# Kernel optimization log

Measured on AMD Instinct MI355X. Metric: run time of the kernel, lower is better.

Reference implementation:

```python
import jax, jax.numpy as jnp
import numpy as np

B, S, H, NH = 8, 1024, 1024, 16
HD = H // NH  # head dim = 64

def setup_inputs() -> dict:
    key = jax.random.key(0)
    ks = jax.random.split(key, 7)
    sc = 0.02
    return {
        "activation": jax.random.normal(ks[0], (B, S, H), jnp.float32),
        "qw": jax.random.normal(ks[1], (H, H), jnp.float32) * sc,
        "qb": jax.random.normal(ks[2], (H,), jnp.float32) * sc,
        "kw": jax.random.normal(ks[3], (H, H), jnp.float32) * sc,
        "kb": jax.random.normal(ks[4], (H,), jnp.float32) * sc,
        "vw": jax.random.normal(ks[5], (H, H), jnp.float32) * sc,
        "vb": jax.random.normal(ks[6], (H,), jnp.float32) * sc,
    }

def reference(activation, qw, qb, kw, kb, vw, vb):
    # QKV projections (torch Linear: x @ W^T + b)
    def proj(x, w, b):
        y = jnp.einsum('bsh,oh->bso', x, w) + b
        # split heads: [B,S,H] -> [B,NH,S,HD]
        return y.reshape(B, S, NH, HD).transpose(0, 2, 1, 3)
    q = proj(activation, qw, qb)
    k = proj(activation, kw, kb)
    v = proj(activation, vw, vb)
    # NOTE: source scales by 1/sqrt(hidden_dim), NOT 1/sqrt(head_dim)
    scale = 1.0 / jnp.sqrt(jnp.float32(H))
    scores = jnp.einsum('bnqd,bnkd->bnqk', q, k) * scale
    probs = jax.nn.softmax(scores, axis=-1)
    ctx = jnp.einsum('bnqk,bnkd->bnqd', probs, v)
    # merge heads: [B,NH,S,HD] -> [B,S,H]
    return ctx.transpose(0, 2, 1, 3).reshape(B, S, H)
```

## Files before the change

kernel.cpp:

```cpp
#include <hip/hip_runtime.h>
#include <cstdint>
#include <cstddef>

#define B_   8
#define S_   1024
#define H_   1024
#define NH_  16
#define HD_  64
#define M_   8192
#define N3_  3072
#define K_   1024

typedef __attribute__((ext_vector_type(8))) short bf16x8;
typedef __attribute__((ext_vector_type(4))) float f32x4;
typedef __attribute__((ext_vector_type(16))) float f32x16;
typedef __attribute__((ext_vector_type(8))) unsigned short u16x8;
typedef __attribute__((ext_vector_type(4))) unsigned u32x4;

__device__ __forceinline__ unsigned short f2bf(float f) {
  unsigned u = __builtin_bit_cast(unsigned, f);
  u += 0x7fffu + ((u >> 16) & 1u);
  return (unsigned short)(u >> 16);
}

__device__ __forceinline__ unsigned cvtpk(float a, float b) {
  unsigned r;
  asm("v_cvt_pk_bf16_f32 %0, %1, %2" : "=v"(r) : "v"(a), "v"(b));
  return r;
}

__global__ void cvt_kernel(const float* __restrict__ src,
                           unsigned short* __restrict__ dst, int n) {
  const int stride = gridDim.x * blockDim.x * 8;
  for (int i = (blockIdx.x * blockDim.x + threadIdx.x) * 8; i < n; i += stride) {
    float4 a = *reinterpret_cast<const float4*>(src + i);
    float4 b = *reinterpret_cast<const float4*>(src + i + 4);
    u16x8 o;
    o[0] = f2bf(a.x); o[1] = f2bf(a.y); o[2] = f2bf(a.z); o[3] = f2bf(a.w);
    o[4] = f2bf(b.x); o[5] = f2bf(b.y); o[6] = f2bf(b.z); o[7] = f2bf(b.w);
    *reinterpret_cast<u16x8*>(dst + i) = o;
  }
}

#define BM 128
#define BN 128
#define BK 64

__global__ __launch_bounds__(256) void qkv_gemm(
    const unsigned short* __restrict__ A,
    const unsigned short* __restrict__ Bw,
    const float* __restrict__ qb, const float* __restrict__ kb,
    const float* __restrict__ vb,
    unsigned short* __restrict__ Qh,
    unsigned short* __restrict__ Kh,
    unsigned short* __restrict__ Vth)
{
  __shared__ unsigned short As[BM * BK];
  __shared__ unsigned short Bs[BN * BK];
  const int t = threadIdx.x;
  const int lane = t & 63;
  const int bm = blockIdx.x, bn = blockIdx.y;
  const int wm = t >> 7, wn = (t >> 6) & 1;

  f32x4 acc[4][4] = {};

  const char* Ab = (const char*)(A + (size_t)bm * BM * K_);
  const char* Bb = (const char*)(Bw + (size_t)bn * BN * K_);

  for (int kt = 0; kt < K_ / BK; ++kt) {
    const int k0b = kt * BK * 2;
    #pragma unroll
    for (int i = 0; i < 4; ++i) {
      const int off = (i * 256 + t) * 16;
      const int row = off >> 7;
      const int c16 = (off >> 4) & 7;
      const int sc  = c16 ^ (row & 7);
      __builtin_amdgcn_global_load_lds(
          (const __attribute__((address_space(1))) void*)(Ab + (size_t)row * (K_ * 2) + k0b + sc * 16),
          (__attribute__((address_space(3))) void*)((char*)As + off), 16, 0, 0);
      __builtin_amdgcn_global_load_lds(
          (const __attribute__((address_space(1))) void*)(Bb + (size_t)row * (K_ * 2) + k0b + sc * 16),
          (__attribute__((address_space(3))) void*)((char*)Bs + off), 16, 0, 0);
    }
    __syncthreads();

    #pragma unroll
    for (int kk = 0; kk < 2; ++kk) {
      bf16x8 af[4], bfr[4];
      #pragma unroll
      for (int mb = 0; mb < 4; ++mb) {
        const int row = wm * 64 + mb * 16 + (lane & 15);
        const int j   = kk * 4 + (lane >> 4);
        af[mb] = *reinterpret_cast<const bf16x8*>(
            (const char*)As + row * 128 + ((j ^ (row & 7)) << 4));
      }
      #pragma unroll
      for (int nb = 0; nb < 4; ++nb) {
        const int row = wn * 64 + nb * 16 + (lane & 15);
        const int j   = kk * 4 + (lane >> 4);
        bfr[nb] = *reinterpret_cast<const bf16x8*>(
            (const char*)Bs + row * 128 + ((j ^ (row & 7)) << 4));
      }
      #pragma unroll
      for (int mb = 0; mb < 4; ++mb)
        #pragma unroll
        for (int nb = 0; nb < 4; ++nb)
          acc[mb][nb] = __builtin_amdgcn_mfma_f32_16x16x32_bf16(
              af[mb], bfr[nb], acc[mb][nb], 0, 0, 0);
    }
    __syncthreads();
  }

  const int grow = bm * BM + wm * 64;
  const int gcol = bn * BN + wn * 64;
  #pragma unroll
  for (int nb = 0; nb < 4; ++nb) {
    const int col = gcol + nb * 16 + (lane & 15);
    const int tensor = col >> 10;
    const int o  = col & 1023;
    const int nh = o >> 6, hd = o & 63;
    const float* bias = (tensor == 0) ? qb : (tensor == 1) ? kb : vb;
    const float bv  = bias[o];
    const float scl = (tensor == 0) ? 0.04508422f : 1.0f;
    #pragma unroll
    for (int mb = 0; mb < 4; ++mb) {
      #pragma unroll
      for (int r = 0; r < 4; ++r) {
        const int i  = grow + mb * 16 + (lane >> 4) * 4 + r;
        const int bb = i >> 10, s = i & 1023;
        const unsigned short h = f2bf((acc[mb][nb][r] + bv) * scl);
        const int bhn = bb * NH_ + nh;
        if (tensor == 0)      Qh[((size_t)bhn * S_ + s) * HD_ + hd] = h;
        else if (tensor == 1) Kh[((size_t)bhn * S_ + s) * HD_ + hd] = h;
        else                  Vth[(size_t)bhn * 65536 + (s >> 6) * 4096 + hd * 64 + (s & 63)] = h;
      }
    }
  }
}

__device__ __forceinline__ bf16x8 mk_frag(const f32x16& s, const int base) {
  unsigned a0 = cvtpk(s[base + 0], s[base + 1]);
  unsigned a1 = cvtpk(s[base + 2], s[base + 3]);
  unsigned b0 = cvtpk(s[base + 4], s[base + 5]);
  unsigned b1 = cvtpk(s[base + 6], s[base + 7]);
  asm("v_permlane32_swap_b32 %0, %1" : "+v"(a0), "+v"(b0));
  asm("v_permlane32_swap_b32 %0, %1" : "+v"(a1), "+v"(b1));
  u32x4 u = {a0, a1, b0, b1};
  return __builtin_bit_cast(bf16x8, u);
}

__global__ __launch_bounds__(256, 3) void attn_kernel(
    const unsigned short* __restrict__ Qh,
    const unsigned short* __restrict__ Kh,
    const unsigned short* __restrict__ Vth,
    float* __restrict__ Out)
{
  __shared__ char sm[2][16384];
  const int t = threadIdx.x;
  const int lane = t & 63;
  const int wave = t >> 6;
  const int l31 = lane & 31;
  const int hi = lane >> 5;
  const int hw = blockIdx.x;
  const int xcd = hw & 7;
  const int qt = (hw >> 3) & 7;
  const int bh = (hw >> 6) * 8 + xcd;
  const int b = bh >> 4, nh = bh & 15;

  const unsigned short* Qp = Qh + (size_t)bh * (S_ * HD_);
  const char* Kp = (const char*)Kh + (size_t)bh * 131072;
  const char* Vp = (const char*)Vth + (size_t)bh * 131072;
  const int q0 = qt * 128 + wave * 32;

  bf16x8 bq[4];
  #pragma unroll
  for (int st = 0; st < 4; ++st)
    bq[st] = *reinterpret_cast<const bf16x8*>(
        Qp + (size_t)(q0 + l31) * HD_ + st * 16 + hi * 8);

  const int soff0 = wave * 1024 + lane * 16;
  #define STAGE_TILE(dstbase, srcbase)                                            \
    _Pragma("unroll")                                                             \
    for (int j = 0; j < 2; ++j) {                                                 \
      const int off = j * 4096 + soff0;                                           \
      const int row = off >> 7;                                                   \
      const int sc  = ((off >> 4) & 7) ^ (row & 7);    \
      __builtin_amdgcn_global_load_lds(                                           \
          (const __attribute__((address_space(1))) void*)((srcbase) + row * 128 + sc * 16), \
          (__attribute__((address_space(3))) void*)((dstbase) + off), 16, 0, 0);  \
    }

  STAGE_TILE(&sm[0][0],    Kp)
  STAGE_TILE(&sm[0][8192], Vp)
  __syncthreads();

  f32x16 o0 = {}, o1 = {};
  float lsum = 0.f;
  const int swr = l31 & 7;

  for (int kt = 0; kt < 16; ++kt) {
    const int cur = kt & 1;
    if (kt < 15) {
      STAGE_TILE(&sm[cur ^ 1][0],    Kp + (kt + 1) * 8192)
      STAGE_TILE(&sm[cur ^ 1][8192], Vp + (kt + 1) * 8192)
    }
    const char* Kb = &sm[cur][0];
    const char* Vb = &sm[cur][8192];

    f32x16 s0 = {}, s1 = {};
    #pragma unroll
    for (int st = 0; st < 4; ++st) {
      const int c = ((st * 2 + hi) ^ swr) << 4;
      bf16x8 ka = *reinterpret_cast<const bf16x8*>(Kb + l31 * 128 + c);
      bf16x8 kc = *reinterpret_cast<const bf16x8*>(Kb + (l31 + 32) * 128 + c);
      s0 = __builtin_amdgcn_mfma_f32_32x32x16_bf16(ka, bq[st], s0, 0, 0, 0);
      s1 = __builtin_amdgcn_mfma_f32_32x32x16_bf16(kc, bq[st], s1, 0, 0, 0);
    }

    bf16x8 va[4];
    #pragma unroll
    for (int ks = 0; ks < 2; ++ks) {
      const int c = ((ks * 2 + hi) ^ swr) << 4;
      va[ks * 2]     = *reinterpret_cast<const bf16x8*>(Vb + l31 * 128 + c);
      va[ks * 2 + 1] = *reinterpret_cast<const bf16x8*>(Vb + (l31 + 32) * 128 + c);
    }
    #pragma unroll
    for (int r = 0; r < 16; ++r) {
      s0[r] = __builtin_amdgcn_exp2f(s0[r]);
      lsum += s0[r];
    }
    bf16x8 f0 = mk_frag(s0, 0);
    bf16x8 f1 = mk_frag(s0, 8);
    o0 = __builtin_amdgcn_mfma_f32_32x32x16_bf16(f0, va[0], o0, 0, 0, 0);
    o1 = __builtin_amdgcn_mfma_f32_32x32x16_bf16(f0, va[1], o1, 0, 0, 0);
    o0 = __builtin_amdgcn_mfma_f32_32x32x16_bf16(f1, va[2], o0, 0, 0, 0);
    o1 = __builtin_amdgcn_mfma_f32_32x32x16_bf16(f1, va[3], o1, 0, 0, 0);

    #pragma unroll
    for (int ks = 0; ks < 2; ++ks) {
      const int c = (((ks + 2) * 2 + hi) ^ swr) << 4;
      va[ks * 2]     = *reinterpret_cast<const bf16x8*>(Vb + l31 * 128 + c);
      va[ks * 2 + 1] = *reinterpret_cast<const bf16x8*>(Vb + (l31 + 32) * 128 + c);
    }
    #pragma unroll
    for (int r = 0; r < 16; ++r) {
      s1[r] = __builtin_amdgcn_exp2f(s1[r]);
      lsum += s1[r];
    }
    bf16x8 f2 = mk_frag(s1, 0);
    bf16x8 f3 = mk_frag(s1, 8);
    o0 = __builtin_amdgcn_mfma_f32_32x32x16_bf16(f2, va[0], o0, 0, 0, 0);
    o1 = __builtin_amdgcn_mfma_f32_32x32x16_bf16(f2, va[1], o1, 0, 0, 0);
    o0 = __builtin_amdgcn_mfma_f32_32x32x16_bf16(f3, va[2], o0, 0, 0, 0);
    o1 = __builtin_amdgcn_mfma_f32_32x32x16_bf16(f3, va[3], o1, 0, 0, 0);

    __syncthreads();
  }

  const float ltot = lsum + __shfl_xor(lsum, 32);
  const float inv = 1.0f / ltot;
  #pragma unroll
  for (int r = 0; r < 16; ++r) {
    const int crow = (r & 3) + 8 * (r >> 2) + 4 * hi;
    const float invq = __shfl(inv, crow);
    float* op = Out + ((size_t)(b * S_ + q0 + crow)) * H_ + nh * HD_ + l31;
    op[0]  = o0[r] * invq;
    op[32] = o1[r] * invq;
  }
}

extern "C" void kernel_launch(void* const* d_in, const int* in_sizes, int n_in,
                              void* d_out, int out_size, void* d_ws, size_t ws_size,
                              hipStream_t stream) {
  const float* act = (const float*)d_in[0];
  const float* qw  = (const float*)d_in[1];
  const float* qb  = (const float*)d_in[2];
  const float* kw  = (const float*)d_in[3];
  const float* kb  = (const float*)d_in[4];
  const float* vw  = (const float*)d_in[5];
  const float* vb  = (const float*)d_in[6];

  char* ws = (char*)d_ws;
  unsigned short* actb = (unsigned short*)ws;
  unsigned short* wb   = (unsigned short*)(ws + 16777216);
  unsigned short* Qh   = (unsigned short*)(ws + 23068672);
  unsigned short* Kh   = Qh + 8388608;
  unsigned short* Vth  = Kh + 8388608;

  cvt_kernel<<<4096, 256, 0, stream>>>(act, actb, M_ * K_);
  cvt_kernel<<<512, 256, 0, stream>>>(qw, wb,               H_ * H_);
  cvt_kernel<<<512, 256, 0, stream>>>(kw, wb + 1048576,     H_ * H_);
  cvt_kernel<<<512, 256, 0, stream>>>(vw, wb + 2097152,     H_ * H_);

  dim3 gg(M_ / BM, N3_ / BN);
  qkv_gemm<<<gg, 256, 0, stream>>>(actb, wb, qb, kb, vb, Qh, Kh, Vth);

  attn_kernel<<<1024, 256, 0, stream>>>(Qh, Kh, Vth, (float*)d_out);
}
```

Before: 141.5 us.

## Rewrite QKV GEMM with 256x256 tiles and double-buffered phased LDS pipeline

The QKV projection GEMM moves from 128x128 tiles with single-buffered LDS and 256 threads to 256x256 tiles computed by 512 threads. It uses 128 KB of dynamic LDS with double buffering. Each k-step is split into four sub-phases that interleave global-to-LDS prefetch of the next tile with MFMA on the current one, using explicit vmcnt waits, barriers and s_setprio. A block-index swizzle groups tiles across XCDs for better L2 reuse. This targets load latency that is exposed and the low reuse of small tiles, at the cost of one block per CU and fragile hand-tuned wait counts.

After: 178.1 us. 25.8% more time.

```diff
diff --git a/kernel.cpp b/kernel.cpp
--- a/kernel.cpp
+++ b/kernel.cpp
@@ -42,11 +42,7 @@
   }
 }
 
-#define BM 128
-#define BN 128
-#define BK 64
-
-__global__ __launch_bounds__(256) void qkv_gemm(
+__global__ __launch_bounds__(512, 2) void qkv_gemm(
     const unsigned short* __restrict__ A,
     const unsigned short* __restrict__ Bw,
     const float* __restrict__ qb, const float* __restrict__ kb,
@@ -55,84 +51,129 @@
     unsigned short* __restrict__ Kh,
     unsigned short* __restrict__ Vth)
 {
-  __shared__ unsigned short As[BM * BK];
-  __shared__ unsigned short Bs[BN * BK];
+  extern __shared__ char sm[];
+  char* Asm = sm;
+  char* Bsm = sm + 65536;
+
   const int t = threadIdx.x;
   const int lane = t & 63;
-  const int bm = blockIdx.x, bn = blockIdx.y;
-  const int wm = t >> 7, wn = (t >> 6) & 1;
-
-  f32x4 acc[4][4] = {};
-
-  const char* Ab = (const char*)(A + (size_t)bm * BM * K_);
-  const char* Bb = (const char*)(Bw + (size_t)bn * BN * K_);
-
-  for (int kt = 0; kt < K_ / BK; ++kt) {
-    const int k0b = kt * BK * 2;
-    #pragma unroll
-    for (int i = 0; i < 4; ++i) {
-      const int off = (i * 256 + t) * 16;
-      const int row = off >> 7;
-      const int c16 = (off >> 4) & 7;
-      const int sc  = c16 ^ (row & 7);
-      __builtin_amdgcn_global_load_lds(
-          (const __attribute__((address_space(1))) void*)(Ab + (size_t)row * (K_ * 2) + k0b + sc * 16),
-          (__attribute__((address_space(3))) void*)((char*)As + off), 16, 0, 0);
-      __builtin_amdgcn_global_load_lds(
-          (const __attribute__((address_space(1))) void*)(Bb + (size_t)row * (K_ * 2) + k0b + sc * 16),
-          (__attribute__((address_space(3))) void*)((char*)Bs + off), 16, 0, 0);
-    }
-    __syncthreads();
-
-    #pragma unroll
-    for (int kk = 0; kk < 2; ++kk) {
-      bf16x8 af[4], bfr[4];
+  const int wave = t >> 6;
+  const int wm = wave >> 2;
+  const int wn = wave & 3;
+
+  const int bid = blockIdx.x;
+  const int swz = (bid & 7) * 48 + (bid >> 3);
+  const int bm = swz & 31;
+  const int bn = swz >> 5;
+
+  const char* Ab = (const char*)A + (size_t)bm * 256 * 2048;
+  const char* Bb = (const char*)Bw + (size_t)bn * 256 * 2048;
+
+  f32x4 acc[2][2][4][2] = {};
+
+  #define STG(lbase, gbase, kt, h)                                             \
+    { _Pragma("unroll")                                                        \
+      for (int j = 0; j < 2; ++j) {                                            \
+        const int off = (h) * 16384 + j * 8192 + t * 16;                       \
+        const int row = off >> 7;                                              \
+        const int sc  = ((off >> 4) & 7) ^ (row & 7);                          \
+        __builtin_amdgcn_global_load_lds(                                      \
+          (const __attribute__((address_space(1))) void*)((gbase) + row * 2048 + (kt) * 128 + sc * 16), \
+          (__attribute__((address_space(3))) void*)((lbase) + off), 16, 0, 0); \
+      } }
+
+  #define VM4 asm volatile("s_waitcnt vmcnt(4)" ::: "memory")
+  #define VM2 asm volatile("s_waitcnt vmcnt(2)" ::: "memory")
+  #define VM0 asm volatile("s_waitcnt vmcnt(0)" ::: "memory")
+  #define BAR asm volatile("s_barrier" ::: "memory")
+  #define NOPS
+
+  #define PHASE(MH, NH, STAGE_STMT, WAIT_STMT)                                 \
+  {                                                                            \
+    bf16x8 afr[2][4], bfr[2][2];                                               \
+    _Pragma("unroll")                                                          \
+    for (int ks = 0; ks < 2; ++ks) {                                           \
+      _Pragma("unroll")                                                        \
+      for (int f = 0; f < 4; ++f) {                                            \
+        const int ar = (MH) * 128 + wm * 64 + f * 16 + (lane & 15);            \
+        afr[ks][f] = *(const bf16x8*)(Acur + ar * 128 +                        \
+                      (((ks * 4 + (lane >> 4)) ^ (ar & 7)) << 4));             \
+      }                                                                        \
+      _Pragma("unroll")                                                        \
+      for (int g = 0; g < 2; ++g) {                                            \
+        const int br = (NH) * 128 + wn * 32 + g * 16 + (lane & 15);            \
+        bfr[ks][g] = *(const bf16x8*)(Bcur + br * 128 +                        \
+                      (((ks * 4 + (lane >> 4)) ^ (br & 7)) << 4));             \
+      }                                                                        \
+    }                                                                          \
+    STAGE_STMT;                                                                \
+    WAIT_STMT;                                                                 \
+    BAR;                                                                       \
+    __builtin_amdgcn_s_setprio(1);                                             \
+    _Pragma("unroll")                                                          \
+    for (int ks = 0; ks < 2; ++ks)                                             \
+      _Pragma("unroll")                                                        \
+      for (int f = 0; f < 4; ++f)                                              \
+        _Pragma("unroll")                                                      \
+        for (int g = 0; g < 2; ++g)                                            \
+          acc[MH][NH][f][g] = __builtin_amdgcn_mfma_f32_16x16x32_bf16(         \
+              afr[ks][f], bfr[ks][g], acc[MH][NH][f][g], 0, 0, 0);             \
+    __builtin_amdgcn_s_setprio(0);                                             \
+    BAR;                                                                       \
+  }
+
+  STG(Asm, Ab, 0, 0)
+  STG(Bsm, Bb, 0, 0)
+  STG(Bsm, Bb, 0, 1)
+  STG(Asm, Ab, 0, 1)
+  VM4;
+  BAR;
+
+  for (int kt = 0; kt < 15; ++kt) {
+    const char* Acur = Asm + (kt & 1) * 32768;
+    const char* Bcur = Bsm + (kt & 1) * 32768;
+    char* Anx = Asm + ((kt + 1) & 1) * 32768;
+    char* Bnx = Bsm + ((kt + 1) & 1) * 32768;
+    PHASE(0, 0, STG(Anx, Ab, kt + 1, 0), VM4)
+    PHASE(0, 1, STG(Bnx, Bb, kt + 1, 0), VM4)
+    PHASE(1, 0, STG(Bnx, Bb, kt + 1, 1), NOPS)
+    PHASE(1, 1, STG(Anx, Ab, kt + 1, 1), VM4)
+  }
+  {
+    const char* Acur = Asm + 32768;
+    const char* Bcur = Bsm + 32768;
+    PHASE(0, 0, NOPS, VM2)
+    PHASE(0, 1, NOPS, VM0)
+    PHASE(1, 0, NOPS, NOPS)
+    PHASE(1, 1, NOPS, NOPS)
+  }
+
+  #pragma unroll
+  for (int mh = 0; mh < 2; ++mh) {
+    #pragma unroll
+    for (int nh = 0; nh < 2; ++nh) {
       #pragma unroll
-      for (int mb = 0; mb < 4; ++mb) {
-        const int row = wm * 64 + mb * 16 + (lane & 15);
-        const int j   = kk * 4 + (lane >> 4);
-        af[mb] = *reinterpret_cast<const bf16x8*>(
-            (const char*)As + row * 128 + ((j ^ (row & 7)) << 4));
-      }
-      #pragma unroll
-      for (int nb = 0; nb < 4; ++nb) {
-        const int row = wn * 64 + nb * 16 + (lane & 15);
-        const int j   = kk * 4 + (lane >> 4);
-        bfr[nb] = *reinterpret_cast<const bf16x8*>(
-            (const char*)Bs + row * 128 + ((j ^ (row & 7)) << 4));
-      }
-      #pragma unroll
-      for (int mb = 0; mb < 4; ++mb)
+      for (int g = 0; g < 2; ++g) {
+        const int col = bn * 256 + nh * 128 + wn * 32 + g * 16 + (lane & 15);
+        const int tensor = col >> 10;
+        const int o  = col & 1023;
+        const int nhh = o >> 6, hd = o & 63;
+        const float* bias = (tensor == 0) ? qb : (tensor == 1) ? kb : vb;
+        const float bv  = bias[o];
+        const float scl = (tensor == 0) ? 0.04508422f : 1.0f;
         #pragma unroll
-        for (int nb = 0; nb < 4; ++nb)
-          acc[mb][nb] = __builtin_amdgcn_mfma_f32_16x16x32_bf16(
-              af[mb], bfr[nb], acc[mb][nb], 0, 0, 0);
-    }
-    __syncthreads();
-  }
-
-  const int grow = bm * BM + wm * 64;
-  const int gcol = bn * BN + wn * 64;
-  #pragma unroll
-  for (int nb = 0; nb < 4; ++nb) {
-    const int col = gcol + nb * 16 + (lane & 15);
-    const int tensor = col >> 10;
-    const int o  = col & 1023;
-    const int nh = o >> 6, hd = o & 63;
-    const float* bias = (tensor == 0) ? qb : (tensor == 1) ? kb : vb;
-    const float bv  = bias[o];
-    const float scl = (tensor == 0) ? 0.04508422f : 1.0f;
-    #pragma unroll
-    for (int mb = 0; mb < 4; ++mb) {
-      #pragma unroll
-      for (int r = 0; r < 4; ++r) {
-        const int i  = grow + mb * 16 + (lane >> 4) * 4 + r;
-        const int bb = i >> 10, s = i & 1023;
-        const unsigned short h = f2bf((acc[mb][nb][r] + bv) * scl);
-        const int bhn = bb * NH_ + nh;
-        if (tensor == 0)      Qh[((size_t)bhn * S_ + s) * HD_ + hd] = h;
-        else if (tensor == 1) Kh[((size_t)bhn * S_ + s) * HD_ + hd] = h;
-        else                  Vth[(size_t)bhn * 65536 + (s >> 6) * 4096 + hd * 64 + (s & 63)] = h;
+        for (int f = 0; f < 4; ++f) {
+          #pragma unroll
+          for (int r = 0; r < 4; ++r) {
+            const int i = bm * 256 + mh * 128 + wm * 64 + f * 16 + (lane >> 4) * 4 + r;
+            const int bb = i >> 10, s = i & 1023;
+            const unsigned short hval = f2bf((acc[mh][nh][f][g][r] + bv) * scl);
+            const int bhn = bb * NH_ + nhh;
+            if (tensor == 0)      Qh[((size_t)bhn * S_ + s) * HD_ + hd] = hval;
+            else if (tensor == 1) Kh[((size_t)bhn * S_ + s) * HD_ + hd] = hval;
+            else                  Vth[(size_t)bhn * 65536 + (s >> 6) * 4096 + hd * 64 + (s & 63)] = hval;
+          }
+        }
       }
     }
   }
@@ -155,7 +196,7 @@
     const unsigned short* __restrict__ Vth,
     float* __restrict__ Out)
 {
-  __shared__ char sm[2][16384];
+  __shared__ char smx[2][16384];
   const int t = threadIdx.x;
   const int lane = t & 63;
   const int wave = t >> 6;
@@ -184,14 +225,14 @@
     for (int j = 0; j < 2; ++j) {                                                 \
       const int off = j * 4096 + soff0;                                           \
       const int row = off >> 7;                                                   \
-      const int sc  = ((off >> 4) & 7) ^ (row & 7);    \
+      const int sc  = ((off >> 4) & 7) ^ (row & 7);                               \
       __builtin_amdgcn_global_load_lds(                                           \
           (const __attribute__((address_space(1))) void*)((srcbase) + row * 128 + sc * 16), \
           (__attribute__((address_space(3))) void*)((dstbase) + off), 16, 0, 0);  \
     }
 
-  STAGE_TILE(&sm[0][0],    Kp)
-  STAGE_TILE(&sm[0][8192], Vp)
+  STAGE_TILE(&smx[0][0],    Kp)
+  STAGE_TILE(&smx[0][8192], Vp)
   __syncthreads();
 
   f32x16 o0 = {}, o1 = {};
@@ -201,11 +242,11 @@
   for (int kt = 0; kt < 16; ++kt) {
     const int cur = kt & 1;
     if (kt < 15) {
-      STAGE_TILE(&sm[cur ^ 1][0],    Kp + (kt + 1) * 8192)
-      STAGE_TILE(&sm[cur ^ 1][8192], Vp + (kt + 1) * 8192)
-    }
-    const char* Kb = &sm[cur][0];
-    const char* Vb = &sm[cur][8192];
+      STAGE_TILE(&smx[cur ^ 1][0],    Kp + (kt + 1) * 8192)
+      STAGE_TILE(&smx[cur ^ 1][8192], Vp + (kt + 1) * 8192)
+    }
+    const char* Kb = &smx[cur][0];
+    const char* Vb = &smx[cur][8192];
 
     f32x16 s0 = {}, s1 = {};
     #pragma unroll
@@ -292,8 +333,9 @@
   cvt_kernel<<<512, 256, 0, stream>>>(kw, wb + 1048576,     H_ * H_);
   cvt_kernel<<<512, 256, 0, stream>>>(vw, wb + 2097152,     H_ * H_);
 
-  dim3 gg(M_ / BM, N3_ / BN);
-  qkv_gemm<<<gg, 256, 0, stream>>>(actb, wb, qb, kb, vb, Qh, Kh, Vth);
+  hipFuncSetAttribute((const void*)qkv_gemm,
+                      hipFuncAttributeMaxDynamicSharedMemorySize, 131072);
+  qkv_gemm<<<384, 512, 131072, stream>>>(actb, wb, qb, kb, vb, Qh, Kh, Vth);
 
   attn_kernel<<<1024, 256, 0, stream>>>(Qh, Kh, Vth, (float*)d_out);
 }
```
